# Kernel optimization log

Hardware: AMD Instinct MI355X
Metric: run time of the kernel (lower is better)

Reference implementation:

```python
import jax, jax.numpy as jnp
import numpy as np

DIM, N_HEAD, DK, DV = 1024, 16, 64, 64
B, S = 1, 4096


def setup_inputs() -> dict:
    key = jax.random.key(0)
    ks = jax.random.split(key, 9)
    sd = 0.02
    return {
        "x": jax.random.normal(ks[0], (B, S, DIM), dtype=jnp.float32),
        "Wq": jax.random.normal(ks[1], (DIM, N_HEAD * DK), dtype=jnp.float32) * sd,
        "bq": jnp.zeros((N_HEAD * DK,), dtype=jnp.float32),
        "Wk": jax.random.normal(ks[2], (DIM, N_HEAD * DK), dtype=jnp.float32) * sd,
        "bk": jnp.zeros((N_HEAD * DK,), dtype=jnp.float32),
        "Wv": jax.random.normal(ks[3], (DIM, N_HEAD * DV), dtype=jnp.float32) * sd,
        "bv": jnp.zeros((N_HEAD * DV,), dtype=jnp.float32),
        "Wo": jax.random.normal(ks[4], (N_HEAD * DV, DIM), dtype=jnp.float32) * sd,
        "bo": jnp.zeros((DIM,), dtype=jnp.float32),
    }


def reference(x, Wq, bq, Wk, bk, Wv, bv, Wo, bo):
    b, s, _ = x.shape
    scale = DK ** (-0.5)
    # projections -> [b, h, s, d]
    q = (x @ Wq + bq).reshape(b, s, N_HEAD, DK).transpose(0, 2, 1, 3)
    k = (x @ Wk + bk).reshape(b, s, N_HEAD, DK).transpose(0, 2, 1, 3)
    v = (x @ Wv + bv).reshape(b, s, N_HEAD, DV).transpose(0, 2, 1, 3)
    attn = jnp.einsum("bhqd,bhkd->bhqk", q, k) * scale  # [b,h,s,s]
    attn = jax.nn.softmax(attn, axis=-1)
    out = jnp.einsum("bhqk,bhkd->bhqd", attn, v)  # [b,h,s,dv]
    out = out.transpose(0, 2, 1, 3).reshape(b, s, N_HEAD * DV)
    return out @ Wo + bo
```

## Files before the change

kernel.cpp:

```cpp
#include <hip/hip_runtime.h>
#include <hip/hip_bf16.h>
#include <hip/hip_fp16.h>

#define SEQ 4096
#define DIM 1024
#define NH 16
#define NT (SEQ / 64)

typedef __attribute__((ext_vector_type(4))) float f32x4;
typedef __attribute__((ext_vector_type(8))) _Float16 half8;
typedef __attribute__((ext_vector_type(4))) _Float16 half4;
typedef __attribute__((ext_vector_type(2))) unsigned uint2v;

#if __has_builtin(__builtin_amdgcn_exp2f)
#define EXP2(x) __builtin_amdgcn_exp2f(x)
#else
#define EXP2(x) exp2f(x)
#endif

#define SMC 0.18033688f


__global__ __launch_bounds__(256) void conv_x(const float* __restrict__ x,
                                              _Float16* __restrict__ xh, int n) {
  int i = (blockIdx.x * 256 + threadIdx.x) * 4;
  if (i >= n) return;
  float4 v = *reinterpret_cast<const float4*>(x + i);
  half4 h;
  h[0] = (_Float16)v.x; h[1] = (_Float16)v.y;
  h[2] = (_Float16)v.z; h[3] = (_Float16)v.w;
  *reinterpret_cast<half4*>(xh + i) = h;
}

__global__ __launch_bounds__(256) void conv_wT4(const float* __restrict__ W0,
                                                const float* __restrict__ W1,
                                                const float* __restrict__ W2,
                                                const float* __restrict__ W3,
                                                _Float16* __restrict__ T0,
                                                _Float16* __restrict__ T1,
                                                _Float16* __restrict__ T2,
                                                _Float16* __restrict__ T3) {
  const float* W = blockIdx.z == 0 ? W0 : blockIdx.z == 1 ? W1 : blockIdx.z == 2 ? W2 : W3;
  _Float16* Wt = blockIdx.z == 0 ? T0 : blockIdx.z == 1 ? T1 : blockIdx.z == 2 ? T2 : T3;
  __shared__ float t[32][33];
  int bx = blockIdx.x * 32;
  int by = blockIdx.y * 32;
  int tx = threadIdx.x & 31, ty = threadIdx.x >> 5;
#pragma unroll
  for (int i = 0; i < 4; i++)
    t[ty + i * 8][tx] = W[(by + ty + i * 8) * DIM + bx + tx];
  __syncthreads();
#pragma unroll
  for (int i = 0; i < 4; i++)
    Wt[(bx + ty + i * 8) * DIM + by + tx] = (_Float16)t[tx][ty + i * 8];
}

template <int MODE>
__device__ __forceinline__ void gemm_body(const _Float16* __restrict__ A,
                                          const _Float16* __restrict__ Bt,
                                          const float* __restrict__ bias,
                                          void* __restrict__ outp,
                                          int M, int N, int Kd, int bmb, int bnb) {
  __shared__ __align__(16) _Float16 As[64][72];
  __shared__ __align__(16) _Float16 Bs[128][72];
  const int tid = threadIdx.x, lane = tid & 63, w = tid >> 6;
  const int bm = bmb * 64, bn = bnb * 128;
  const int l15 = lane & 15, g = lane >> 4, kb = g * 8;
  const int sra = tid >> 2, sca = (tid & 3) * 16;
  const int srb = tid >> 1, scb = (tid & 1) * 32;
  f32x4 acc[4][2] = {};

  uint4 ar0, ar1, br0, br1, br2, br3;
  auto LOADT = [&](int k0) {
    const _Float16* ap = A + (size_t)(bm + sra) * Kd + k0 + sca;
    ar0 = *reinterpret_cast<const uint4*>(ap);
    ar1 = *reinterpret_cast<const uint4*>(ap + 8);
    const _Float16* bp = Bt + (size_t)(bn + srb) * Kd + k0 + scb;
    br0 = *reinterpret_cast<const uint4*>(bp);
    br1 = *reinterpret_cast<const uint4*>(bp + 8);
    br2 = *reinterpret_cast<const uint4*>(bp + 16);
    br3 = *reinterpret_cast<const uint4*>(bp + 24);
  };

  LOADT(0);
  for (int k0 = 0; k0 < Kd; k0 += 64) {
    __syncthreads();
    *reinterpret_cast<uint4*>(&As[sra][sca]) = ar0;
    *reinterpret_cast<uint4*>(&As[sra][sca + 8]) = ar1;
    *reinterpret_cast<uint4*>(&Bs[srb][scb]) = br0;
    *reinterpret_cast<uint4*>(&Bs[srb][scb + 8]) = br1;
    *reinterpret_cast<uint4*>(&Bs[srb][scb + 16]) = br2;
    *reinterpret_cast<uint4*>(&Bs[srb][scb + 24]) = br3;
    __syncthreads();
    if (k0 + 64 < Kd) LOADT(k0 + 64);
#pragma unroll
    for (int kk = 0; kk < 64; kk += 32) {
      half8 af[4], bf[2];
#pragma unroll
      for (int i = 0; i < 4; i++)
        af[i] = *reinterpret_cast<const half8*>(&As[i * 16 + l15][kk + kb]);
#pragma unroll
      for (int j = 0; j < 2; j++)
        bf[j] = *reinterpret_cast<const half8*>(&Bs[w * 32 + j * 16 + l15][kk + kb]);
      __builtin_amdgcn_s_setprio(1);
#pragma unroll
      for (int i = 0; i < 4; i++)
#pragma unroll
        for (int j = 0; j < 2; j++)
          acc[i][j] = __builtin_amdgcn_mfma_f32_16x16x32_f16(af[i], bf[j], acc[i][j], 0, 0, 0);
      __builtin_amdgcn_s_setprio(0);
    }
  }

#pragma unroll
  for (int i = 0; i < 4; i++)
#pragma unroll
    for (int j = 0; j < 2; j++) {
      const int row0 = bm + i * 16 + g * 4;
      const int col = bn + w * 32 + j * 16 + l15;
      if (MODE == 2) {
        half4 hv;
#pragma unroll
        for (int r = 0; r < 4; r++) hv[r] = (_Float16)(acc[i][j][r] + bias[col]);
        *reinterpret_cast<half4*>(&((_Float16*)outp)[(size_t)col * M + row0]) = hv;
      } else {
#pragma unroll
        for (int r = 0; r < 4; r++) {
          float vv = acc[i][j][r] + bias[col];
          if (MODE == 0) {
            _Float16* O = (_Float16*)outp;
            O[(((col >> 6) * SEQ) + row0 + r) * 64 + (col & 63)] = (_Float16)vv;
          } else {
            float* O = (float*)outp;
            O[(size_t)(row0 + r) * N + col] = vv;
          }
        }
      }
    }
}

__global__ __launch_bounds__(256) void gemm_qkv(const _Float16* __restrict__ A,
                                                const _Float16* __restrict__ WqT,
                                                const _Float16* __restrict__ WkT,
                                                const _Float16* __restrict__ WvT,
                                                const float* __restrict__ bq,
                                                const float* __restrict__ bk,
                                                const float* __restrict__ bv,
                                                _Float16* __restrict__ Qd,
                                                _Float16* __restrict__ Kd,
                                                _Float16* __restrict__ Vd) {
  if (blockIdx.z == 0)
    gemm_body<0>(A, WqT, bq, (void*)Qd, SEQ, DIM, DIM, blockIdx.x, blockIdx.y);
  else if (blockIdx.z == 1)
    gemm_body<0>(A, WkT, bk, (void*)Kd, SEQ, DIM, DIM, blockIdx.x, blockIdx.y);
  else
    gemm_body<2>(A, WvT, bv, (void*)Vd, SEQ, DIM, DIM, blockIdx.x, blockIdx.y);
}

__global__ __launch_bounds__(256) void gemm_out(const _Float16* __restrict__ A,
                                                const _Float16* __restrict__ Bt,
                                                const float* __restrict__ bias,
                                                float* __restrict__ out) {
  gemm_body<1>(A, Bt, bias, (void*)out, SEQ, DIM, DIM, blockIdx.x, blockIdx.y);
}

__global__ __launch_bounds__(256) void attn_fwd(const _Float16* __restrict__ Q,
                                                const _Float16* __restrict__ Kh,
                                                const _Float16* __restrict__ Vt_g,
                                                _Float16* __restrict__ Og) {
  __shared__ __align__(16) _Float16 Ks[3][64][72];
  __shared__ __align__(16) _Float16 Vs[3][64][72];
  const int h = blockIdx.y;
  const int q0 = blockIdx.x * 128;
  const int tid = threadIdx.x, lane = tid & 63, w = tid >> 6;
  const int l15 = lane & 15, g = lane >> 4, kb = g * 8;

  const int qrow = q0 + w * 32 + l15;
  const _Float16* qp = Q + ((size_t)h * SEQ + qrow) * 64;
  half8 qf[2][2];
  qf[0][0] = *reinterpret_cast<const half8*>(qp + kb);
  qf[0][1] = *reinterpret_cast<const half8*>(qp + 32 + kb);
  qf[1][0] = *reinterpret_cast<const half8*>(qp + 16 * 64 + kb);
  qf[1][1] = *reinterpret_cast<const half8*>(qp + 16 * 64 + 32 + kb);

  f32x4 o[2][4] = {};
  float m[2] = {-1e30f, -1e30f};
  float lsum[2] = {0.f, 0.f};
  float negmC[2] = {1e30f, 1e30f};

  const int srow = tid >> 3, sc8 = (tid & 7) * 8;
  const _Float16* kbase = Kh + (size_t)h * SEQ * 64;
  const _Float16* vbase = Vt_g + (size_t)h * 64 * SEQ;

  uint4 kr0, kr1, vr0, vr1;
  auto LOADKV = [&](int kt2) {
    const _Float16* kp = kbase + (size_t)(kt2 * 64 + srow) * 64 + sc8;
    kr0 = *reinterpret_cast<const uint4*>(kp);
    kr1 = *reinterpret_cast<const uint4*>(kp + 32 * 64);
    const _Float16* vp = vbase + (size_t)srow * SEQ + kt2 * 64 + sc8;
    vr0 = *reinterpret_cast<const uint4*>(vp);
    vr1 = *reinterpret_cast<const uint4*>(vp + 32 * SEQ);
  };
  auto STAGE = [&](int buf) {
    *reinterpret_cast<uint4*>(&Ks[buf][srow][sc8]) = kr0;
    *reinterpret_cast<uint4*>(&Ks[buf][srow + 32][sc8]) = kr1;
    *reinterpret_cast<uint4*>(&Vs[buf][srow][sc8]) = vr0;
    *reinterpret_cast<uint4*>(&Vs[buf][srow + 32][sc8]) = vr1;
  };

  auto QK = [&](int tile, f32x4 (&sf)[2][4]) {
    const int b = tile % 3;
    __builtin_amdgcn_s_setprio(1);
#pragma unroll
    for (int f = 0; f < 4; f++) {
      half8 kf0 = *reinterpret_cast<const half8*>(&Ks[b][f * 16 + l15][kb]);
      half8 kf1 = *reinterpret_cast<const half8*>(&Ks[b][f * 16 + l15][32 + kb]);
      sf[0][f] = __builtin_amdgcn_mfma_f32_16x16x32_f16(kf0, qf[0][0], sf[0][f], 0, 0, 0);
      sf[0][f] = __builtin_amdgcn_mfma_f32_16x16x32_f16(kf1, qf[0][1], sf[0][f], 0, 0, 0);
      sf[1][f] = __builtin_amdgcn_mfma_f32_16x16x32_f16(kf0, qf[1][0], sf[1][f], 0, 0, 0);
      sf[1][f] = __builtin_amdgcn_mfma_f32_16x16x32_f16(kf1, qf[1][1], sf[1][f], 0, 0, 0);
    }
    __builtin_amdgcn_s_setprio(0);
  };

  auto ITER = [&](int t, f32x4 (&scur)[2][4], f32x4 (&snext)[2][4]) {
    if (t + 1 < NT) {
#pragma unroll
      for (int s = 0; s < 2; s++)
#pragma unroll
        for (int f = 0; f < 4; f++) snext[s][f] = (f32x4){0.f, 0.f, 0.f, 0.f};
      QK(t + 1, snext);
    }

    half4 pb[2][4];
#pragma unroll
    for (int s = 0; s < 2; s++) {
      float pm = fmaxf(fmaxf(fmaxf(scur[s][0][0], scur[s][0][1]), fmaxf(scur[s][0][2], scur[s][0][3])),
                       fmaxf(fmaxf(scur[s][1][0], scur[s][1][1]), fmaxf(scur[s][1][2], scur[s][1][3])));
      pm = fmaxf(pm, fmaxf(fmaxf(fmaxf(scur[s][2][0], scur[s][2][1]), fmaxf(scur[s][2][2], scur[s][2][3])),
                           fmaxf(fmaxf(scur[s][3][0], scur[s][3][1]), fmaxf(scur[s][3][2], scur[s][3][3]))));
      if (__any(pm > m[s] + 64.f)) {
        pm = fmaxf(pm, __shfl_xor(pm, 16, 64));
        pm = fmaxf(pm, __shfl_xor(pm, 32, 64));
        float mn = fmaxf(m[s], pm);
        float al = EXP2((m[s] - mn) * SMC);
        m[s] = mn;
        negmC[s] = -mn * SMC;
        lsum[s] *= al;
#pragma unroll
        for (int f = 0; f < 4; f++) o[s][f] *= al;
      }
#pragma unroll
      for (int f = 0; f < 4; f++) {
        float p0 = EXP2(fmaf(scur[s][f][0], SMC, negmC[s]));
        float p1 = EXP2(fmaf(scur[s][f][1], SMC, negmC[s]));
        float p2 = EXP2(fmaf(scur[s][f][2], SMC, negmC[s]));
        float p3 = EXP2(fmaf(scur[s][f][3], SMC, negmC[s]));
        lsum[s] += (p0 + p1) + (p2 + p3);
        auto h01 = __builtin_amdgcn_cvt_pkrtz(p0, p1);
        auto h23 = __builtin_amdgcn_cvt_pkrtz(p2, p3);
        uint2v uu = {__builtin_bit_cast(unsigned, h01), __builtin_bit_cast(unsigned, h23)};
        pb[s][f] = __builtin_bit_cast(half4, uu);
      }
    }

    const int bv = t % 3;
    __builtin_amdgcn_s_setprio(1);
#pragma unroll
    for (int fv = 0; fv < 4; fv++) {
#pragma unroll
      for (int fk = 0; fk < 4; fk++) {
        half4 va = *reinterpret_cast<const half4*>(&Vs[bv][fv * 16 + l15][fk * 16 + g * 4]);
        o[0][fv] = __builtin_amdgcn_mfma_f32_16x16x16f16(va, pb[0][fk], o[0][fv], 0, 0, 0);
        o[1][fv] = __builtin_amdgcn_mfma_f32_16x16x16f16(va, pb[1][fk], o[1][fv], 0, 0, 0);
      }
    }
    __builtin_amdgcn_s_setprio(0);

    if (t + 2 < NT) STAGE((t + 2) % 3);
    if (t + 3 < NT) LOADKV(t + 3);
    __syncthreads();
  };

  LOADKV(0); STAGE(0);
  LOADKV(1); STAGE(1);
  LOADKV(2);
  __syncthreads();

  f32x4 sfA[2][4] = {}, sfB[2][4] = {};
  QK(0, sfA);
  for (int t = 0; t < NT; t += 2) {
    ITER(t, sfA, sfB);
    ITER(t + 1, sfB, sfA);
  }

#pragma unroll
  for (int s = 0; s < 2; s++) {
    float ls = lsum[s];
    ls += __shfl_xor(ls, 16, 64);
    ls += __shfl_xor(ls, 32, 64);
    float rinv = 1.f / ls;
#pragma unroll
    for (int f = 0; f < 4; f++) {
      half4 hv;
#pragma unroll
      for (int r = 0; r < 4; r++) hv[r] = (_Float16)(o[s][f][r] * rinv);
      *reinterpret_cast<half4*>(
          &Og[(size_t)(qrow + 16 * s) * DIM + h * 64 + f * 16 + g * 4]) = hv;
    }
  }
}


extern "C" void kernel_launch(void* const* d_in, const int* in_sizes, int n_in,
                              void* d_out, int out_size, void* d_ws, size_t ws_size,
                              hipStream_t stream) {
  const float* x  = (const float*)d_in[0];
  const float* Wq = (const float*)d_in[1];
  const float* bq = (const float*)d_in[2];
  const float* Wk = (const float*)d_in[3];
  const float* bk = (const float*)d_in[4];
  const float* Wv = (const float*)d_in[5];
  const float* bv = (const float*)d_in[6];
  const float* Wo = (const float*)d_in[7];
  const float* bo = (const float*)d_in[8];

  char* ws = (char*)d_ws;
  _Float16* xh  = (_Float16*)ws;
  _Float16* WqT = (_Float16*)(ws + (size_t)SEQ * DIM * 2);
  _Float16* WkT = WqT + DIM * DIM;
  _Float16* WvT = WkT + DIM * DIM;
  _Float16* WoT = WvT + DIM * DIM;
  _Float16* Qd  = WoT + DIM * DIM;
  _Float16* Kd  = Qd + (size_t)SEQ * DIM;
  _Float16* Vd  = Kd + (size_t)SEQ * DIM;
  _Float16* Od  = Vd + (size_t)SEQ * DIM;

  conv_x<<<(SEQ * DIM) / 1024, 256, 0, stream>>>(x, xh, SEQ * DIM);
  conv_wT4<<<dim3(32, 32, 4), 256, 0, stream>>>(Wq, Wk, Wv, Wo, WqT, WkT, WvT, WoT);

  gemm_qkv<<<dim3(SEQ / 64, DIM / 128, 3), 256, 0, stream>>>(
      xh, WqT, WkT, WvT, bq, bk, bv, Qd, Kd, Vd);

  attn_fwd<<<dim3(SEQ / 128, NH), 256, 0, stream>>>(Qd, Kd, Vd, Od);

  gemm_out<<<dim3(SEQ / 64, DIM / 128), 256, 0, stream>>>(Od, WoT, bo, (float*)d_out);
}
```

Measured before the change: 185.8 us.

## Load K fragments directly into registers and compute row sums via MFMA

Measured after the change: 368.7 us. 98.4% more time.

```diff
diff --git a/kernel.cpp b/kernel.cpp
--- a/kernel.cpp
+++ b/kernel.cpp
@@ -168,7 +168,6 @@
                                                 const _Float16* __restrict__ Kh,
                                                 const _Float16* __restrict__ Vt_g,
                                                 _Float16* __restrict__ Og) {
-  __shared__ __align__(16) _Float16 Ks[3][64][72];
   __shared__ __align__(16) _Float16 Vs[3][64][72];
   const int h = blockIdx.y;
   const int q0 = blockIdx.x * 128;
@@ -184,53 +183,56 @@
   qf[1][1] = *reinterpret_cast<const half8*>(qp + 16 * 64 + 32 + kb);
 
   f32x4 o[2][4] = {};
+  f32x4 ol[2] = {};
   float m[2] = {-1e30f, -1e30f};
-  float lsum[2] = {0.f, 0.f};
   float negmC[2] = {1e30f, 1e30f};
 
   const int srow = tid >> 3, sc8 = (tid & 7) * 8;
   const _Float16* kbase = Kh + (size_t)h * SEQ * 64;
   const _Float16* vbase = Vt_g + (size_t)h * 64 * SEQ;
 
-  uint4 kr0, kr1, vr0, vr1;
-  auto LOADKV = [&](int kt2) {
-    const _Float16* kp = kbase + (size_t)(kt2 * 64 + srow) * 64 + sc8;
-    kr0 = *reinterpret_cast<const uint4*>(kp);
-    kr1 = *reinterpret_cast<const uint4*>(kp + 32 * 64);
+  const f32x4 kZero = {0.f, 0.f, 0.f, 0.f};
+  const _Float16 one1 = (_Float16)1.f;
+  const half4 kOnes = {one1, one1, one1, one1};
+
+  half8 kA[4][2], kB[4][2];
+  uint4 vrA0, vrA1, vrB0, vrB1;
+
+  auto LOADK = [&](int kt2, half8 (&kr)[4][2]) {
+#pragma unroll
+    for (int f = 0; f < 4; f++) {
+      const _Float16* kp = kbase + (size_t)(kt2 * 64 + f * 16 + l15) * 64 + kb;
+      kr[f][0] = *reinterpret_cast<const half8*>(kp);
+      kr[f][1] = *reinterpret_cast<const half8*>(kp + 32);
+    }
+  };
+  auto LOADV = [&](int kt2, uint4& v0, uint4& v1) {
     const _Float16* vp = vbase + (size_t)srow * SEQ + kt2 * 64 + sc8;
-    vr0 = *reinterpret_cast<const uint4*>(vp);
-    vr1 = *reinterpret_cast<const uint4*>(vp + 32 * SEQ);
-  };
-  auto STAGE = [&](int buf) {
-    *reinterpret_cast<uint4*>(&Ks[buf][srow][sc8]) = kr0;
-    *reinterpret_cast<uint4*>(&Ks[buf][srow + 32][sc8]) = kr1;
-    *reinterpret_cast<uint4*>(&Vs[buf][srow][sc8]) = vr0;
-    *reinterpret_cast<uint4*>(&Vs[buf][srow + 32][sc8]) = vr1;
-  };
-
-  auto QK = [&](int tile, f32x4 (&sf)[2][4]) {
-    const int b = tile % 3;
+    v0 = *reinterpret_cast<const uint4*>(vp);
+    v1 = *reinterpret_cast<const uint4*>(vp + 32 * SEQ);
+  };
+  auto STAGEV = [&](int buf, const uint4& v0, const uint4& v1) {
+    *reinterpret_cast<uint4*>(&Vs[buf][srow][sc8]) = v0;
+    *reinterpret_cast<uint4*>(&Vs[buf][srow + 32][sc8]) = v1;
+  };
+  auto QK = [&](const half8 (&kr)[4][2], f32x4 (&sf)[2][4]) {
     __builtin_amdgcn_s_setprio(1);
 #pragma unroll
     for (int f = 0; f < 4; f++) {
-      half8 kf0 = *reinterpret_cast<const half8*>(&Ks[b][f * 16 + l15][kb]);
-      half8 kf1 = *reinterpret_cast<const half8*>(&Ks[b][f * 16 + l15][32 + kb]);
-      sf[0][f] = __builtin_amdgcn_mfma_f32_16x16x32_f16(kf0, qf[0][0], sf[0][f], 0, 0, 0);
-      sf[0][f] = __builtin_amdgcn_mfma_f32_16x16x32_f16(kf1, qf[0][1], sf[0][f], 0, 0, 0);
-      sf[1][f] = __builtin_amdgcn_mfma_f32_16x16x32_f16(kf0, qf[1][0], sf[1][f], 0, 0, 0);
-      sf[1][f] = __builtin_amdgcn_mfma_f32_16x16x32_f16(kf1, qf[1][1], sf[1][f], 0, 0, 0);
+      sf[0][f] = __builtin_amdgcn_mfma_f32_16x16x32_f16(kr[f][0], qf[0][0], kZero, 0, 0, 0);
+      sf[0][f] = __builtin_amdgcn_mfma_f32_16x16x32_f16(kr[f][1], qf[0][1], sf[0][f], 0, 0, 0);
+      sf[1][f] = __builtin_amdgcn_mfma_f32_16x16x32_f16(kr[f][0], qf[1][0], kZero, 0, 0, 0);
+      sf[1][f] = __builtin_amdgcn_mfma_f32_16x16x32_f16(kr[f][1], qf[1][1], sf[1][f], 0, 0, 0);
     }
     __builtin_amdgcn_s_setprio(0);
   };
 
-  auto ITER = [&](int t, f32x4 (&scur)[2][4], f32x4 (&snext)[2][4]) {
-    if (t + 1 < NT) {
-#pragma unroll
-      for (int s = 0; s < 2; s++)
-#pragma unroll
-        for (int f = 0; f < 4; f++) snext[s][f] = (f32x4){0.f, 0.f, 0.f, 0.f};
-      QK(t + 1, snext);
-    }
+  auto ITER = [&](int t, f32x4 (&scur)[2][4], f32x4 (&snext)[2][4],
+                  half8 (&kCur)[4][2], half8 (&kNxt)[4][2],
+                  uint4& vC0, uint4& vC1, uint4& vN0, uint4& vN1) {
+    if (t + 2 < NT) LOADK(t + 2, kNxt);
+    if (t + 3 < NT) LOADV(t + 3, vN0, vN1);
+    if (t + 1 < NT) QK(kCur, snext);
 
     half4 pb[2][4];
 #pragma unroll
@@ -246,7 +248,7 @@
         float al = EXP2((m[s] - mn) * SMC);
         m[s] = mn;
         negmC[s] = -mn * SMC;
-        lsum[s] *= al;
+        ol[s] *= al;
 #pragma unroll
         for (int f = 0; f < 4; f++) o[s][f] *= al;
       }
@@ -256,7 +258,6 @@
         float p1 = EXP2(fmaf(scur[s][f][1], SMC, negmC[s]));
         float p2 = EXP2(fmaf(scur[s][f][2], SMC, negmC[s]));
         float p3 = EXP2(fmaf(scur[s][f][3], SMC, negmC[s]));
-        lsum[s] += (p0 + p1) + (p2 + p3);
         auto h01 = __builtin_amdgcn_cvt_pkrtz(p0, p1);
         auto h23 = __builtin_amdgcn_cvt_pkrtz(p2, p3);
         uint2v uu = {__builtin_bit_cast(unsigned, h01), __builtin_bit_cast(unsigned, h23)};
@@ -267,39 +268,41 @@
     const int bv = t % 3;
     __builtin_amdgcn_s_setprio(1);
 #pragma unroll
-    for (int fv = 0; fv < 4; fv++) {
+    for (int fv = 0; fv < 4; fv++)
 #pragma unroll
       for (int fk = 0; fk < 4; fk++) {
         half4 va = *reinterpret_cast<const half4*>(&Vs[bv][fv * 16 + l15][fk * 16 + g * 4]);
         o[0][fv] = __builtin_amdgcn_mfma_f32_16x16x16f16(va, pb[0][fk], o[0][fv], 0, 0, 0);
         o[1][fv] = __builtin_amdgcn_mfma_f32_16x16x16f16(va, pb[1][fk], o[1][fv], 0, 0, 0);
       }
+#pragma unroll
+    for (int fk = 0; fk < 4; fk++) {
+      ol[0] = __builtin_amdgcn_mfma_f32_16x16x16f16(kOnes, pb[0][fk], ol[0], 0, 0, 0);
+      ol[1] = __builtin_amdgcn_mfma_f32_16x16x16f16(kOnes, pb[1][fk], ol[1], 0, 0, 0);
     }
     __builtin_amdgcn_s_setprio(0);
 
-    if (t + 2 < NT) STAGE((t + 2) % 3);
-    if (t + 3 < NT) LOADKV(t + 3);
+    if (t + 2 < NT) STAGEV((t + 2) % 3, vC0, vC1);
     __syncthreads();
   };
 
-  LOADKV(0); STAGE(0);
-  LOADKV(1); STAGE(1);
-  LOADKV(2);
+  LOADV(0, vrA0, vrA1); STAGEV(0, vrA0, vrA1);
+  LOADV(1, vrA0, vrA1); STAGEV(1, vrA0, vrA1);
+  LOADK(0, kA);
+  LOADK(1, kB);
+  LOADV(2, vrA0, vrA1);
   __syncthreads();
 
-  f32x4 sfA[2][4] = {}, sfB[2][4] = {};
-  QK(0, sfA);
+  f32x4 sfA[2][4], sfB[2][4];
+  QK(kA, sfA);
   for (int t = 0; t < NT; t += 2) {
-    ITER(t, sfA, sfB);
-    ITER(t + 1, sfB, sfA);
+    ITER(t, sfA, sfB, kB, kA, vrA0, vrA1, vrB0, vrB1);
+    ITER(t + 1, sfB, sfA, kA, kB, vrB0, vrB1, vrA0, vrA1);
   }
 
 #pragma unroll
   for (int s = 0; s < 2; s++) {
-    float ls = lsum[s];
-    ls += __shfl_xor(ls, 16, 64);
-    ls += __shfl_xor(ls, 32, 64);
-    float rinv = 1.f / ls;
+    float rinv = 1.f / ol[s][0];
 #pragma unroll
     for (int f = 0; f < 4; f++) {
       half4 hv;
```

## Route P through LDS to use 16x16x32 MFMA for PV and row sums

Applied to the files above, without the earlier changes.

Result: faster. 177.0 us (-4.8%).

```diff
diff --git a/kernel.cpp b/kernel.cpp
--- a/kernel.cpp
+++ b/kernel.cpp
@@ -170,6 +170,7 @@
                                                 _Float16* __restrict__ Og) {
   __shared__ __align__(16) _Float16 Ks[3][64][72];
   __shared__ __align__(16) _Float16 Vs[3][64][72];
+  __shared__ __align__(16) _Float16 Ps[4][2][16][72];
   const int h = blockIdx.y;
   const int q0 = blockIdx.x * 128;
   const int tid = threadIdx.x, lane = tid & 63, w = tid >> 6;
@@ -184,9 +185,13 @@
   qf[1][1] = *reinterpret_cast<const half8*>(qp + 16 * 64 + 32 + kb);
 
   f32x4 o[2][4] = {};
+  f32x4 ol[2] = {};
   float m[2] = {-1e30f, -1e30f};
-  float lsum[2] = {0.f, 0.f};
   float negmC[2] = {1e30f, 1e30f};
+
+  const f32x4 kZero = {0.f, 0.f, 0.f, 0.f};
+  const _Float16 one1 = (_Float16)1.f;
+  const half8 kOnes8 = {one1, one1, one1, one1, one1, one1, one1, one1};
 
   const int srow = tid >> 3, sc8 = (tid & 7) * 8;
   const _Float16* kbase = Kh + (size_t)h * SEQ * 64;
@@ -215,30 +220,25 @@
     for (int f = 0; f < 4; f++) {
       half8 kf0 = *reinterpret_cast<const half8*>(&Ks[b][f * 16 + l15][kb]);
       half8 kf1 = *reinterpret_cast<const half8*>(&Ks[b][f * 16 + l15][32 + kb]);
-      sf[0][f] = __builtin_amdgcn_mfma_f32_16x16x32_f16(kf0, qf[0][0], sf[0][f], 0, 0, 0);
+      sf[0][f] = __builtin_amdgcn_mfma_f32_16x16x32_f16(kf0, qf[0][0], kZero, 0, 0, 0);
       sf[0][f] = __builtin_amdgcn_mfma_f32_16x16x32_f16(kf1, qf[0][1], sf[0][f], 0, 0, 0);
-      sf[1][f] = __builtin_amdgcn_mfma_f32_16x16x32_f16(kf0, qf[1][0], sf[1][f], 0, 0, 0);
+      sf[1][f] = __builtin_amdgcn_mfma_f32_16x16x32_f16(kf0, qf[1][0], kZero, 0, 0, 0);
       sf[1][f] = __builtin_amdgcn_mfma_f32_16x16x32_f16(kf1, qf[1][1], sf[1][f], 0, 0, 0);
     }
     __builtin_amdgcn_s_setprio(0);
   };
 
   auto ITER = [&](int t, f32x4 (&scur)[2][4], f32x4 (&snext)[2][4]) {
-    if (t + 1 < NT) {
-#pragma unroll
-      for (int s = 0; s < 2; s++)
-#pragma unroll
-        for (int f = 0; f < 4; f++) snext[s][f] = (f32x4){0.f, 0.f, 0.f, 0.f};
-      QK(t + 1, snext);
-    }
-
-    half4 pb[2][4];
+    if (t + 1 < NT) QK(t + 1, snext);
+
 #pragma unroll
     for (int s = 0; s < 2; s++) {
-      float pm = fmaxf(fmaxf(fmaxf(scur[s][0][0], scur[s][0][1]), fmaxf(scur[s][0][2], scur[s][0][3])),
-                       fmaxf(fmaxf(scur[s][1][0], scur[s][1][1]), fmaxf(scur[s][1][2], scur[s][1][3])));
-      pm = fmaxf(pm, fmaxf(fmaxf(fmaxf(scur[s][2][0], scur[s][2][1]), fmaxf(scur[s][2][2], scur[s][2][3])),
-                           fmaxf(fmaxf(scur[s][3][0], scur[s][3][1]), fmaxf(scur[s][3][2], scur[s][3][3]))));
+      float m0 = fmaxf(fmaxf(scur[s][0][0], scur[s][0][1]), scur[s][0][2]);
+      float m1 = fmaxf(fmaxf(scur[s][0][3], scur[s][1][0]), scur[s][1][1]);
+      float m2 = fmaxf(fmaxf(scur[s][1][2], scur[s][1][3]), scur[s][2][0]);
+      float m3 = fmaxf(fmaxf(scur[s][2][1], scur[s][2][2]), scur[s][2][3]);
+      float m4 = fmaxf(fmaxf(scur[s][3][0], scur[s][3][1]), scur[s][3][2]);
+      float pm = fmaxf(fmaxf(fmaxf(m0, m1), m2), fmaxf(fmaxf(m3, m4), scur[s][3][3]));
       if (__any(pm > m[s] + 64.f)) {
         pm = fmaxf(pm, __shfl_xor(pm, 16, 64));
         pm = fmaxf(pm, __shfl_xor(pm, 32, 64));
@@ -246,7 +246,7 @@
         float al = EXP2((m[s] - mn) * SMC);
         m[s] = mn;
         negmC[s] = -mn * SMC;
-        lsum[s] *= al;
+        ol[s] *= al;
 #pragma unroll
         for (int f = 0; f < 4; f++) o[s][f] *= al;
       }
@@ -256,25 +256,36 @@
         float p1 = EXP2(fmaf(scur[s][f][1], SMC, negmC[s]));
         float p2 = EXP2(fmaf(scur[s][f][2], SMC, negmC[s]));
         float p3 = EXP2(fmaf(scur[s][f][3], SMC, negmC[s]));
-        lsum[s] += (p0 + p1) + (p2 + p3);
         auto h01 = __builtin_amdgcn_cvt_pkrtz(p0, p1);
         auto h23 = __builtin_amdgcn_cvt_pkrtz(p2, p3);
         uint2v uu = {__builtin_bit_cast(unsigned, h01), __builtin_bit_cast(unsigned, h23)};
-        pb[s][f] = __builtin_bit_cast(half4, uu);
+        *reinterpret_cast<half4*>(&Ps[w][s][l15][f * 16 + g * 4]) =
+            __builtin_bit_cast(half4, uu);
       }
+    }
+
+    half8 pa[2][2];
+#pragma unroll
+    for (int s = 0; s < 2; s++) {
+      pa[s][0] = *reinterpret_cast<const half8*>(&Ps[w][s][l15][kb]);
+      pa[s][1] = *reinterpret_cast<const half8*>(&Ps[w][s][l15][32 + kb]);
     }
 
     const int bv = t % 3;
     __builtin_amdgcn_s_setprio(1);
 #pragma unroll
-    for (int fv = 0; fv < 4; fv++) {
-#pragma unroll
-      for (int fk = 0; fk < 4; fk++) {
-        half4 va = *reinterpret_cast<const half4*>(&Vs[bv][fv * 16 + l15][fk * 16 + g * 4]);
-        o[0][fv] = __builtin_amdgcn_mfma_f32_16x16x16f16(va, pb[0][fk], o[0][fv], 0, 0, 0);
-        o[1][fv] = __builtin_amdgcn_mfma_f32_16x16x16f16(va, pb[1][fk], o[1][fv], 0, 0, 0);
-      }
-    }
+    for (int f = 0; f < 4; f++) {
+      half8 vf0 = *reinterpret_cast<const half8*>(&Vs[bv][f * 16 + l15][kb]);
+      half8 vf1 = *reinterpret_cast<const half8*>(&Vs[bv][f * 16 + l15][32 + kb]);
+      o[0][f] = __builtin_amdgcn_mfma_f32_16x16x32_f16(vf0, pa[0][0], o[0][f], 0, 0, 0);
+      o[0][f] = __builtin_amdgcn_mfma_f32_16x16x32_f16(vf1, pa[0][1], o[0][f], 0, 0, 0);
+      o[1][f] = __builtin_amdgcn_mfma_f32_16x16x32_f16(vf0, pa[1][0], o[1][f], 0, 0, 0);
+      o[1][f] = __builtin_amdgcn_mfma_f32_16x16x32_f16(vf1, pa[1][1], o[1][f], 0, 0, 0);
+    }
+    ol[0] = __builtin_amdgcn_mfma_f32_16x16x32_f16(kOnes8, pa[0][0], ol[0], 0, 0, 0);
+    ol[0] = __builtin_amdgcn_mfma_f32_16x16x32_f16(kOnes8, pa[0][1], ol[0], 0, 0, 0);
+    ol[1] = __builtin_amdgcn_mfma_f32_16x16x32_f16(kOnes8, pa[1][0], ol[1], 0, 0, 0);
+    ol[1] = __builtin_amdgcn_mfma_f32_16x16x32_f16(kOnes8, pa[1][1], ol[1], 0, 0, 0);
     __builtin_amdgcn_s_setprio(0);
 
     if (t + 2 < NT) STAGE((t + 2) % 3);
@@ -287,7 +298,7 @@
   LOADKV(2);
   __syncthreads();
 
-  f32x4 sfA[2][4] = {}, sfB[2][4] = {};
+  f32x4 sfA[2][4], sfB[2][4];
   QK(0, sfA);
   for (int t = 0; t < NT; t += 2) {
     ITER(t, sfA, sfB);
@@ -296,10 +307,7 @@
 
 #pragma unroll
   for (int s = 0; s < 2; s++) {
-    float ls = lsum[s];
-    ls += __shfl_xor(ls, 16, 64);
-    ls += __shfl_xor(ls, 32, 64);
-    float rinv = 1.f / ls;
+    float rinv = 1.f / ol[s][0];
 #pragma unroll
     for (int f = 0; f < 4; f++) {
       half4 hv;
```
